# Optimization experiments

Measured on AMD Instinct MI355X. Metric: run time of the kernel, lower is better.

## Reference

```python
import jax, jax.numpy as jnp
import numpy as np

WBITS = 4
GROUP_SIZE = 64
QMAX = 2 ** WBITS - 1  # 15
EPS = 1e-5


def setup_inputs() -> dict:
    key = jax.random.key(0)
    k1, k2, k3 = jax.random.split(key, 3)
    x = jax.random.normal(k1, (1, 512, 11008), dtype=jnp.float32)
    weight = jax.random.normal(k2, (4096, 11008), dtype=jnp.float32) * 0.02
    bias = jax.random.normal(k3, (4096,), dtype=jnp.float32) * 0.02
    return {"x": x, "weight": weight, "bias": bias}


def fake_quant_groupwise(w: jnp.ndarray) -> jnp.ndarray:
    """Uniform affine (asymmetric) group-wise fake quantization of the weight.

    Groups of GROUP_SIZE contiguous elements along the flattened weight share
    one (scale, zero_point) pair, computed dynamically from min/max per group,
    as in UniformAffineQuantizer(wbits, group_size, weight).
    """
    orig_shape = w.shape
    wg = w.reshape(-1, GROUP_SIZE)                     # [n_groups, G]
    xmin = jnp.min(wg, axis=1, keepdims=True)          # [n_groups, 1]
    xmax = jnp.max(wg, axis=1, keepdims=True)
    scale = jnp.maximum(xmax - xmin, EPS) / QMAX       # [n_groups, 1]
    zero_point = jnp.round(-xmin / scale)              # [n_groups, 1]
    w_int = jnp.clip(jnp.round(wg / scale) + zero_point, 0, QMAX)
    w_dq = (w_int - zero_point) * scale
    return w_dq.reshape(orig_shape)


def reference(x, weight, bias):
    w_q = fake_quant_groupwise(weight)                 # [out, in]
    # F.linear: x @ w_q.T + bias
    out = jnp.einsum('bsi,oi->bso', x, w_q) + bias
    return out
```

## Files before the change

kernel.cpp:

```cpp
#include <hip/hip_runtime.h>
#include <hip/hip_bf16.h>
#include <stdint.h>

typedef __attribute__((ext_vector_type(8))) short bf16x8;
typedef __attribute__((ext_vector_type(8))) short short8;
typedef __attribute__((ext_vector_type(4))) float f32x4;

#define M_DIM 512
#define N_DIM 4096
#define K_DIM 11008
#define KSTEPS 172

#define GLOBAL_AS(p) ((const __attribute__((address_space(1))) void*)(p))
#define LDS_AS(p)    ((__attribute__((address_space(3))) void*)(p))

__device__ __forceinline__ short f2bf(float f) {
    unsigned u = __float_as_uint(f);
    unsigned r = u + 0x7fff + ((u >> 16) & 1);
    return (short)(r >> 16);
}

__device__ __forceinline__ unsigned cvt_pk_bf16(float lo, float hi) {
    unsigned r;
    asm("v_cvt_pk_bf16_f32 %0, %1, %2" : "=v"(r) : "v"(lo), "v"(hi));
    return r;
}

__device__ __forceinline__ float dpp_xor1(float v) {
    return __int_as_float(__builtin_amdgcn_mov_dpp(__float_as_int(v), 0xB1, 0xf, 0xf, true));
}
__device__ __forceinline__ float dpp_xor2(float v) {
    return __int_as_float(__builtin_amdgcn_mov_dpp(__float_as_int(v), 0x4E, 0xf, 0xf, true));
}

__device__ __forceinline__ void fence_bar() {
    asm volatile("" ::: "memory");
    __builtin_amdgcn_s_barrier();
    asm volatile("" ::: "memory");
}
#define LGKM0() asm volatile("s_waitcnt lgkmcnt(0)" ::: "memory")
#define VMCNT(n) asm volatile("s_waitcnt vmcnt(" #n ")" ::: "memory")

__global__ __launch_bounds__(256) void conv_x(const float* __restrict__ x, short* __restrict__ xb) {
    const long long total = (long long)M_DIM * K_DIM;
    for (long long e0 = ((long long)blockIdx.x * 256 + threadIdx.x) * 8;
         e0 < total;
         e0 += (long long)gridDim.x * 256 * 8) {
        const float4* p = (const float4*)(x + e0);
        float4 v0 = p[0];
        float4 v1 = p[1];
        short8 s;
        s[0] = f2bf(v0.x); s[1] = f2bf(v0.y); s[2] = f2bf(v0.z); s[3] = f2bf(v0.w);
        s[4] = f2bf(v1.x); s[5] = f2bf(v1.y); s[6] = f2bf(v1.z); s[7] = f2bf(v1.w);
        *(short8*)(xb + e0) = s;
    }
}

__global__ __launch_bounds__(512, 2) void gemm_fq(const short* __restrict__ A,
                                                  const float* __restrict__ W,
                                                  unsigned short* __restrict__ P,
                                                  int spb) {
    __shared__ short As[2][256 * 64];
    __shared__ short Bs[2][256 * 64];
    const int tid  = threadIdx.x;
    const int lane = tid & 63;
    const int w    = tid >> 6;
    const int wr   = w >> 2;
    const int wc   = w & 3;
    const int m0   = blockIdx.y * 256;
    const int n0   = blockIdx.x * 256;
    const int kt0  = blockIdx.z * spb;
    const int kt1  = min(kt0 + spb, KSTEPS);

    const int srow = tid >> 3;
    const int sswz = (tid & 7) ^ (srow & 7);
    const int rC   = tid >> 2;
    const int qC   = tid & 3;
    const int arow = wr * 128 + (lane & 15);
    const int brow = wc * 64 + (lane & 15);
    const int qb   = lane >> 4;

    f32x4  acc[8][4] = {};
    float4 C0[4], C1[4];

    auto stageA = [&](int d, int h, int kt) {
        #pragma unroll
        for (int l = 0; l < 2; ++l) {
            __builtin_amdgcn_global_load_lds(
                GLOBAL_AS(A + (size_t)(m0 + h * 128 + l * 64 + srow) * K_DIM + kt * 64 + sswz * 8),
                LDS_AS(&As[d][(h * 128 + l * 64 + w * 8) * 64]), 16, 0, 0);
        }
    };
    auto loadC = [&](float4 (&dst)[4], int c, int kt) {
        const float4* src = (const float4*)(W + (size_t)(n0 + c * 128 + rC) * K_DIM + (size_t)kt * 64 + qC * 16);
        #pragma unroll
        for (int j = 0; j < 4; ++j) dst[j] = src[j];
    };
    auto quantC = [&](const float4 (&v)[4], int c, short* BsF) {
        const float* pv = (const float*)&v[0];
        float mns[8], mxs[8];
        #pragma unroll
        for (int j = 0; j < 8; ++j) {
            mns[j] = fminf(pv[2 * j], pv[2 * j + 1]);
            mxs[j] = fmaxf(pv[2 * j], pv[2 * j + 1]);
        }
        #pragma unroll
        for (int st = 4; st >= 1; st >>= 1)
            #pragma unroll
            for (int j = 0; j < st; ++j) {
                mns[j] = fminf(mns[j], mns[j + st]);
                mxs[j] = fmaxf(mxs[j], mxs[j + st]);
            }
        float mn = fminf(mns[0], dpp_xor1(mns[0]));
        mn = fminf(mn, dpp_xor2(mn));
        float mx = fmaxf(mxs[0], dpp_xor1(mxs[0]));
        mx = fmaxf(mx, dpp_xor2(mx));
        float range = fmaxf(mx - mn, 1e-5f);
        float scale = range * (1.0f / 15.0f);
        float rs    = 1.0f / scale;
        const int r    = c * 128 + rC;
        const int base = r * 64;
        #pragma unroll
        for (int s4 = 0; s4 < 2; ++s4) {
            float q[8];
            #pragma unroll
            for (int j = 0; j < 8; ++j)
                q[j] = rintf(pv[s4 * 8 + j] * rs) * scale;
            union { unsigned u[4]; short8 s; } pk;
            #pragma unroll
            for (int j = 0; j < 4; ++j)
                pk.u[j] = cvt_pk_bf16(q[2 * j], q[2 * j + 1]);
            const int s = qC * 2 + s4;
            *(short8*)&BsF[base + ((s ^ (r & 7)) * 8)] = pk.s;
        }
    };

    loadC(C0, 0, kt0);
    loadC(C1, 1, kt0);
    stageA(0, 0, kt0);
    stageA(0, 1, kt0);
    VMCNT(8);  quantC(C0, 0, Bs[0]);
    VMCNT(4);  quantC(C1, 1, Bs[0]);
    loadC(C0, 0, kt0 + 1);
    loadC(C1, 1, kt0 + 1);
    VMCNT(8);
    LGKM0();
    fence_bar();

    int par = 0;
    for (int t = kt0; t < kt1; ++t) {
        const int tn  = (t + 1 < kt1) ? t + 1 : t;
        const int tn2 = (t + 2 < kt1) ? t + 2 : kt1 - 1;
        const short* Asc = As[par];
        const short* Bsc = Bs[par];
        short* Bsn = Bs[par ^ 1];

        stageA(par ^ 1, 0, tn);
        stageA(par ^ 1, 1, tn);

        bf16x8 bfr[2][4];
        #pragma unroll
        for (int ks = 0; ks < 2; ++ks)
            #pragma unroll
            for (int fn = 0; fn < 4; ++fn) {
                const int r = brow + fn * 16;
                bfr[ks][fn] = *(const bf16x8*)&Bsc[r * 64 + (((ks * 4 + qb) ^ (r & 7)) * 8)];
            }
        #pragma unroll
        for (int qd = 0; qd < 4; ++qd) {
            bf16x8 af[2][2];
            #pragma unroll
            for (int ks = 0; ks < 2; ++ks)
                #pragma unroll
                for (int j = 0; j < 2; ++j) {
                    const int r = arow + (qd * 2 + j) * 16;
                    af[ks][j] = *(const bf16x8*)&Asc[r * 64 + (((ks * 4 + qb) ^ (r & 7)) * 8)];
                }
            #pragma unroll
            for (int ks = 0; ks < 2; ++ks)
                #pragma unroll
                for (int j = 0; j < 2; ++j)
                    #pragma unroll
                    for (int fn = 0; fn < 4; ++fn)
                        acc[qd * 2 + j][fn] = __builtin_amdgcn_mfma_f32_16x16x32_bf16(
                            af[ks][j], bfr[ks][fn], acc[qd * 2 + j][fn], 0, 0, 0);
        }
        quantC(C0, 0, Bsn);
        quantC(C1, 1, Bsn);
        loadC(C0, 0, tn2);
        loadC(C1, 1, tn2);
        VMCNT(8);
        LGKM0();
        fence_bar();
        par ^= 1;
    }

    VMCNT(0);

    unsigned short* out = P + (size_t)blockIdx.z * M_DIM * N_DIM;
    #pragma unroll
    for (int fm = 0; fm < 8; ++fm) {
        #pragma unroll
        for (int fn = 0; fn < 4; ++fn) {
            const int col  = n0 + wc * 64 + fn * 16 + (lane & 15);
            const int rowb = m0 + wr * 128 + fm * 16 + (lane >> 4) * 4;
            #pragma unroll
            for (int r = 0; r < 4; ++r) {
                out[(size_t)(rowb + r) * N_DIM + col] = (unsigned short)f2bf(acc[fm][fn][r]);
            }
        }
    }
}

__global__ __launch_bounds__(256) void reduce_out(const unsigned short* __restrict__ P,
                                                  const float* __restrict__ bias,
                                                  float* __restrict__ out,
                                                  int splitk) {
    const size_t total = (size_t)M_DIM * N_DIM;
    for (size_t idx8 = ((size_t)blockIdx.x * 256 + threadIdx.x) * 8;
         idx8 < total;
         idx8 += (size_t)gridDim.x * 256 * 8) {
        const int col = (int)(idx8 % N_DIM);
        float s[8];
        {
            float4 b0 = *(const float4*)(bias + col);
            float4 b1 = *(const float4*)(bias + col + 4);
            s[0] = b0.x; s[1] = b0.y; s[2] = b0.z; s[3] = b0.w;
            s[4] = b1.x; s[5] = b1.y; s[6] = b1.z; s[7] = b1.w;
        }
        for (int sp = 0; sp < splitk; ++sp) {
            short8 p = *(const short8*)(P + (size_t)sp * total + idx8);
            #pragma unroll
            for (int j = 0; j < 8; ++j)
                s[j] += __uint_as_float(((unsigned)(unsigned short)p[j]) << 16);
        }
        float4 o0 = {s[0], s[1], s[2], s[3]};
        float4 o1 = {s[4], s[5], s[6], s[7]};
        *(float4*)(out + idx8) = o0;
        *(float4*)(out + idx8 + 4) = o1;
    }
}

extern "C" void kernel_launch(void* const* d_in, const int* in_sizes, int n_in,
                              void* d_out, int out_size, void* d_ws, size_t ws_size,
                              hipStream_t stream) {
    const float* x    = (const float*)d_in[0];
    const float* wgt  = (const float*)d_in[1];
    const float* bias = (const float*)d_in[2];
    float* out = (float*)d_out;

    char* ws = (char*)d_ws;
    const size_t xb_bytes = (size_t)M_DIM * K_DIM * 2;
    short* xb = (short*)ws;
    unsigned short* part = (unsigned short*)(ws + xb_bytes);

    const size_t per_split = (size_t)M_DIM * N_DIM * 2;
    size_t avail = (ws_size > xb_bytes) ? (ws_size - xb_bytes) : 0;
    int splitk = 1, spb = KSTEPS;
    for (int sk = 8; sk >= 1; --sk) {
        if ((size_t)sk * per_split > avail) continue;
        int s = (KSTEPS + sk - 1) / sk;
        int last = KSTEPS - (sk - 1) * s;
        if (last < 2) continue;
        splitk = sk; spb = s;
        break;
    }

    hipLaunchKernelGGL(conv_x, dim3(2048), dim3(256), 0, stream, x, xb);
    hipLaunchKernelGGL(gemm_fq, dim3(N_DIM / 256, M_DIM / 256, splitk), dim3(512), 0, stream,
                       xb, wgt, part, spb);
    hipLaunchKernelGGL(reduce_out, dim3(1024), dim3(256), 0, stream, part, bias, out, splitk);
}
```

Measured before the change: 92.36 us.

## Shrink GEMM tile to 256x128 with 256 threads and single-buffered B

Reduces the block tile from 256x256 to 256x128 and the block from 512 to 256 threads, so each block handles half the output columns, and doubles the grid in N. B in LDS is now single-buffered, with an extra barrier after the MFMA phase before the quantized weights are written. The aim is to cut LDS use and raise occupancy or wave count. In exchange, the A tile is re-read twice as often and the added barrier serialises quantization behind compute.

```diff
diff --git a/kernel.cpp b/kernel.cpp
--- a/kernel.cpp
+++ b/kernel.cpp
@@ -56,24 +56,24 @@
     }
 }
 
-__global__ __launch_bounds__(512, 2) void gemm_fq(const short* __restrict__ A,
+__global__ __launch_bounds__(256, 2) void gemm_fq(const short* __restrict__ A,
                                                   const float* __restrict__ W,
                                                   unsigned short* __restrict__ P,
                                                   int spb) {
     __shared__ short As[2][256 * 64];
-    __shared__ short Bs[2][256 * 64];
+    __shared__ short Bs[128 * 64];
     const int tid  = threadIdx.x;
     const int lane = tid & 63;
     const int w    = tid >> 6;
-    const int wr   = w >> 2;
-    const int wc   = w & 3;
+    const int wr   = w >> 1;
+    const int wc   = w & 1;
     const int m0   = blockIdx.y * 256;
-    const int n0   = blockIdx.x * 256;
+    const int n0   = blockIdx.x * 128;
     const int kt0  = blockIdx.z * spb;
     const int kt1  = min(kt0 + spb, KSTEPS);
 
-    const int srow = tid >> 3;
-    const int sswz = (tid & 7) ^ (srow & 7);
+    const int srow = lane >> 3;
+    const int sswz = (lane & 7) ^ srow;
     const int rC   = tid >> 2;
     const int qC   = tid & 3;
     const int arow = wr * 128 + (lane & 15);
@@ -83,20 +83,21 @@
     f32x4  acc[8][4] = {};
     float4 C0[4], C1[4];
 
-    auto stageA = [&](int d, int h, int kt) {
-        #pragma unroll
-        for (int l = 0; l < 2; ++l) {
+    auto stageA = [&](int d, int kt) {
+        #pragma unroll
+        for (int i = 0; i < 8; ++i) {
+            const int rb = w * 64 + i * 8;
             __builtin_amdgcn_global_load_lds(
-                GLOBAL_AS(A + (size_t)(m0 + h * 128 + l * 64 + srow) * K_DIM + kt * 64 + sswz * 8),
-                LDS_AS(&As[d][(h * 128 + l * 64 + w * 8) * 64]), 16, 0, 0);
+                GLOBAL_AS(A + (size_t)(m0 + rb + srow) * K_DIM + kt * 64 + sswz * 8),
+                LDS_AS(&As[d][rb * 64]), 16, 0, 0);
         }
     };
     auto loadC = [&](float4 (&dst)[4], int c, int kt) {
-        const float4* src = (const float4*)(W + (size_t)(n0 + c * 128 + rC) * K_DIM + (size_t)kt * 64 + qC * 16);
+        const float4* src = (const float4*)(W + (size_t)(n0 + c * 64 + rC) * K_DIM + (size_t)kt * 64 + qC * 16);
         #pragma unroll
         for (int j = 0; j < 4; ++j) dst[j] = src[j];
     };
-    auto quantC = [&](const float4 (&v)[4], int c, short* BsF) {
+    auto quantC = [&](const float4 (&v)[4], int c) {
         const float* pv = (const float*)&v[0];
         float mns[8], mxs[8];
         #pragma unroll
@@ -118,7 +119,7 @@
         float range = fmaxf(mx - mn, 1e-5f);
         float scale = range * (1.0f / 15.0f);
         float rs    = 1.0f / scale;
-        const int r    = c * 128 + rC;
+        const int r    = c * 64 + rC;
         const int base = r * 64;
         #pragma unroll
         for (int s4 = 0; s4 < 2; ++s4) {
@@ -131,16 +132,15 @@
             for (int j = 0; j < 4; ++j)
                 pk.u[j] = cvt_pk_bf16(q[2 * j], q[2 * j + 1]);
             const int s = qC * 2 + s4;
-            *(short8*)&BsF[base + ((s ^ (r & 7)) * 8)] = pk.s;
+            *(short8*)&Bs[base + ((s ^ (r & 7)) * 8)] = pk.s;
         }
     };
 
     loadC(C0, 0, kt0);
     loadC(C1, 1, kt0);
-    stageA(0, 0, kt0);
-    stageA(0, 1, kt0);
-    VMCNT(8);  quantC(C0, 0, Bs[0]);
-    VMCNT(4);  quantC(C1, 1, Bs[0]);
+    stageA(0, kt0);
+    VMCNT(12); quantC(C0, 0);
+    VMCNT(8);  quantC(C1, 1);
     loadC(C0, 0, kt0 + 1);
     loadC(C1, 1, kt0 + 1);
     VMCNT(8);
@@ -152,11 +152,8 @@
         const int tn  = (t + 1 < kt1) ? t + 1 : t;
         const int tn2 = (t + 2 < kt1) ? t + 2 : kt1 - 1;
         const short* Asc = As[par];
-        const short* Bsc = Bs[par];
-        short* Bsn = Bs[par ^ 1];
-
-        stageA(par ^ 1, 0, tn);
-        stageA(par ^ 1, 1, tn);
+
+        stageA(par ^ 1, tn);
 
         bf16x8 bfr[2][4];
         #pragma unroll
@@ -164,7 +161,7 @@
             #pragma unroll
             for (int fn = 0; fn < 4; ++fn) {
                 const int r = brow + fn * 16;
-                bfr[ks][fn] = *(const bf16x8*)&Bsc[r * 64 + (((ks * 4 + qb) ^ (r & 7)) * 8)];
+                bfr[ks][fn] = *(const bf16x8*)&Bs[r * 64 + (((ks * 4 + qb) ^ (r & 7)) * 8)];
             }
         #pragma unroll
         for (int qd = 0; qd < 4; ++qd) {
@@ -185,8 +182,12 @@
                         acc[qd * 2 + j][fn] = __builtin_amdgcn_mfma_f32_16x16x32_bf16(
                             af[ks][j], bfr[ks][fn], acc[qd * 2 + j][fn], 0, 0, 0);
         }
-        quantC(C0, 0, Bsn);
-        quantC(C1, 1, Bsn);
+        fence_bar();
+
+        VMCNT(12);
+        quantC(C0, 0);
+        VMCNT(8);
+        quantC(C1, 1);
         loadC(C0, 0, tn2);
         loadC(C1, 1, tn2);
         VMCNT(8);
@@ -267,7 +268,7 @@
     }
 
     hipLaunchKernelGGL(conv_x, dim3(2048), dim3(256), 0, stream, x, xb);
-    hipLaunchKernelGGL(gemm_fq, dim3(N_DIM / 256, M_DIM / 256, splitk), dim3(512), 0, stream,
+    hipLaunchKernelGGL(gemm_fq, dim3(N_DIM / 128, M_DIM / 256, splitk), dim3(256), 0, stream,
                        xb, wgt, part, spb);
     hipLaunchKernelGGL(reduce_out, dim3(1024), dim3(256), 0, stream, part, bias, out, splitk);
 }
```

New measurement: 87.97 us. 1.05x faster.

## Switch GEMM to 64-column tiles with A fragments read directly from global

Applied to the files above, without the earlier changes.

Shrinks the block tile from 256x256 to a full-M (512) by 64-column tile with 256 threads, and stops staging A in LDS. Each wave now loads its A fragments straight from global memory, and only the quantized weight tile goes through LDS. The intent is to cut LDS footprint and the A staging cost. In exchange, A has no reuse through LDS, every A load is an uncoalesced global read in the MFMA loop, and the weight prefetch no longer waits on vmcnt before quantizing. It also leaves a stray no-op statement behind.

```diff
diff --git a/kernel.cpp b/kernel.cpp
--- a/kernel.cpp
+++ b/kernel.cpp
@@ -10,9 +10,6 @@
 #define N_DIM 4096
 #define K_DIM 11008
 #define KSTEPS 172
-
-#define GLOBAL_AS(p) ((const __attribute__((address_space(1))) void*)(p))
-#define LDS_AS(p)    ((__attribute__((address_space(3))) void*)(p))
 
 __device__ __forceinline__ short f2bf(float f) {
     unsigned u = __float_as_uint(f);
@@ -56,48 +53,34 @@
     }
 }
 
-__global__ __launch_bounds__(512, 2) void gemm_fq(const short* __restrict__ A,
+__global__ __launch_bounds__(256, 2) void gemm_fq(const short* __restrict__ A,
                                                   const float* __restrict__ W,
                                                   unsigned short* __restrict__ P,
                                                   int spb) {
-    __shared__ short As[2][256 * 64];
-    __shared__ short Bs[2][256 * 64];
+    __shared__ short Bs[2][64 * 64];
     const int tid  = threadIdx.x;
     const int lane = tid & 63;
     const int w    = tid >> 6;
-    const int wr   = w >> 2;
-    const int wc   = w & 3;
-    const int m0   = blockIdx.y * 256;
-    const int n0   = blockIdx.x * 256;
+    const int n0   = blockIdx.x * 64;
     const int kt0  = blockIdx.z * spb;
     const int kt1  = min(kt0 + spb, KSTEPS);
 
-    const int srow = tid >> 3;
-    const int sswz = (tid & 7) ^ (srow & 7);
-    const int rC   = tid >> 2;
+    const int rQ   = tid >> 2;
     const int qC   = tid & 3;
-    const int arow = wr * 128 + (lane & 15);
-    const int brow = wc * 64 + (lane & 15);
+    const int arow = w * 128 + (lane & 15);
+    const int brow = lane & 15;
     const int qb   = lane >> 4;
 
     f32x4  acc[8][4] = {};
-    float4 C0[4], C1[4];
-
-    auto stageA = [&](int d, int h, int kt) {
-        #pragma unroll
-        for (int l = 0; l < 2; ++l) {
-            __builtin_amdgcn_global_load_lds(
-                GLOBAL_AS(A + (size_t)(m0 + h * 128 + l * 64 + srow) * K_DIM + kt * 64 + sswz * 8),
-                LDS_AS(&As[d][(h * 128 + l * 64 + w * 8) * 64]), 16, 0, 0);
-        }
+    float4 R[4];
+
+    auto loadR = [&](int kt) {
+        const float4* src = (const float4*)(W + (size_t)(n0 + rQ) * K_DIM + (size_t)kt * 64 + qC * 16);
+        #pragma unroll
+        for (int j = 0; j < 4; ++j) R[j] = src[j];
     };
-    auto loadC = [&](float4 (&dst)[4], int c, int kt) {
-        const float4* src = (const float4*)(W + (size_t)(n0 + c * 128 + rC) * K_DIM + (size_t)kt * 64 + qC * 16);
-        #pragma unroll
-        for (int j = 0; j < 4; ++j) dst[j] = src[j];
-    };
-    auto quantC = [&](const float4 (&v)[4], int c, short* BsF) {
-        const float* pv = (const float*)&v[0];
+    auto quantR = [&](short* BsF) {
+        const float* pv = (const float*)&R[0];
         float mns[8], mxs[8];
         #pragma unroll
         for (int j = 0; j < 8; ++j) {
@@ -118,8 +101,7 @@
         float range = fmaxf(mx - mn, 1e-5f);
         float scale = range * (1.0f / 15.0f);
         float rs    = 1.0f / scale;
-        const int r    = c * 128 + rC;
-        const int base = r * 64;
+        const int base = rQ * 64;
         #pragma unroll
         for (int s4 = 0; s4 < 2; ++s4) {
             float q[8];
@@ -131,32 +113,23 @@
             for (int j = 0; j < 4; ++j)
                 pk.u[j] = cvt_pk_bf16(q[2 * j], q[2 * j + 1]);
             const int s = qC * 2 + s4;
-            *(short8*)&BsF[base + ((s ^ (r & 7)) * 8)] = pk.s;
+            *(short8*)&Bs[0][0] ;
+            *(short8*)&BsF[base + ((s ^ (rQ & 7)) * 8)] = pk.s;
         }
     };
 
-    loadC(C0, 0, kt0);
-    loadC(C1, 1, kt0);
-    stageA(0, 0, kt0);
-    stageA(0, 1, kt0);
-    VMCNT(8);  quantC(C0, 0, Bs[0]);
-    VMCNT(4);  quantC(C1, 1, Bs[0]);
-    loadC(C0, 0, kt0 + 1);
-    loadC(C1, 1, kt0 + 1);
-    VMCNT(8);
+    loadR(kt0);
+    VMCNT(0);
+    quantR(Bs[0]);
+    loadR(kt0 + 1);
     LGKM0();
     fence_bar();
 
     int par = 0;
     for (int t = kt0; t < kt1; ++t) {
-        const int tn  = (t + 1 < kt1) ? t + 1 : t;
         const int tn2 = (t + 2 < kt1) ? t + 2 : kt1 - 1;
-        const short* Asc = As[par];
         const short* Bsc = Bs[par];
         short* Bsn = Bs[par ^ 1];
-
-        stageA(par ^ 1, 0, tn);
-        stageA(par ^ 1, 1, tn);
 
         bf16x8 bfr[2][4];
         #pragma unroll
@@ -173,8 +146,8 @@
             for (int ks = 0; ks < 2; ++ks)
                 #pragma unroll
                 for (int j = 0; j < 2; ++j) {
-                    const int r = arow + (qd * 2 + j) * 16;
-                    af[ks][j] = *(const bf16x8*)&Asc[r * 64 + (((ks * 4 + qb) ^ (r & 7)) * 8)];
+                    const int row = arow + (qd * 2 + j) * 16;
+                    af[ks][j] = *(const bf16x8*)(A + (size_t)row * K_DIM + (size_t)t * 64 + (ks * 4 + qb) * 8);
                 }
             #pragma unroll
             for (int ks = 0; ks < 2; ++ks)
@@ -185,11 +158,9 @@
                         acc[qd * 2 + j][fn] = __builtin_amdgcn_mfma_f32_16x16x32_bf16(
                             af[ks][j], bfr[ks][fn], acc[qd * 2 + j][fn], 0, 0, 0);
         }
-        quantC(C0, 0, Bsn);
-        quantC(C1, 1, Bsn);
-        loadC(C0, 0, tn2);
-        loadC(C1, 1, tn2);
-        VMCNT(8);
+
+        quantR(Bsn);
+        loadR(tn2);
         LGKM0();
         fence_bar();
         par ^= 1;
@@ -202,8 +173,8 @@
     for (int fm = 0; fm < 8; ++fm) {
         #pragma unroll
         for (int fn = 0; fn < 4; ++fn) {
-            const int col  = n0 + wc * 64 + fn * 16 + (lane & 15);
-            const int rowb = m0 + wr * 128 + fm * 16 + (lane >> 4) * 4;
+            const int col  = n0 + fn * 16 + (lane & 15);
+            const int rowb = w * 128 + fm * 16 + (lane >> 4) * 4;
             #pragma unroll
             for (int r = 0; r < 4; ++r) {
                 out[(size_t)(rowb + r) * N_DIM + col] = (unsigned short)f2bf(acc[fm][fn][r]);
@@ -267,7 +238,7 @@
     }
 
     hipLaunchKernelGGL(conv_x, dim3(2048), dim3(256), 0, stream, x, xb);
-    hipLaunchKernelGGL(gemm_fq, dim3(N_DIM / 256, M_DIM / 256, splitk), dim3(512), 0, stream,
+    hipLaunchKernelGGL(gemm_fq, dim3(N_DIM / 64, 1, splitk), dim3(256), 0, stream,
                        xb, wgt, part, spb);
     hipLaunchKernelGGL(reduce_out, dim3(1024), dim3(256), 0, stream, part, bias, out, splitk);
 }
```

New measurement: 115.8 us. 1.25x slower.
